# Optimization experiments

Measured on AMD Instinct MI355X. Metric: run time of the kernel, lower is better.

The kernel has to match this reference:

```python
import jax, jax.numpy as jnp
import numpy as np

H_SIZE = 2048
N_HEADS = 16
N_KV = 4
HEAD_DIM = 128
EPS = 1e-6
ROPE_THETA = 10000.0


def _rms_norm(x, w):
    # per-head RMSNorm over last dim (head_dim)
    var = jnp.mean(jnp.square(x), axis=-1, keepdims=True)
    return x * jax.lax.rsqrt(var + EPS) * w


def _rope(x, positions):
    # neox-style rotary over full head_dim. x: [B,S,H,D], positions: [B,S]
    d = x.shape[-1]
    inv_freq = 1.0 / (ROPE_THETA ** (jnp.arange(0, d, 2, dtype=jnp.float32) / d))
    ang = positions.astype(jnp.float32)[..., None] * inv_freq  # [B,S,D/2]
    cos = jnp.cos(ang)[:, :, None, :]
    sin = jnp.sin(ang)[:, :, None, :]
    x1, x2 = x[..., : d // 2], x[..., d // 2 :]
    return jnp.concatenate([x1 * cos - x2 * sin, x2 * cos + x1 * sin], axis=-1)


def setup_inputs() -> dict:
    key = jax.random.key(0)
    k1, k2, k3 = jax.random.split(key, 3)
    B, S = 2, 2048
    positions = jnp.broadcast_to(jnp.arange(S, dtype=jnp.int32), (B, S))
    hidden_states = jax.random.normal(k1, (B, S, H_SIZE), dtype=jnp.float32)
    w_qkv = jax.random.normal(k2, (H_SIZE, (N_HEADS + 2 * N_KV) * HEAD_DIM), dtype=jnp.float32) * 0.02
    w_o = jax.random.normal(k3, (N_HEADS * HEAD_DIM, H_SIZE), dtype=jnp.float32) * 0.02
    q_norm_w = jnp.ones((HEAD_DIM,), dtype=jnp.float32)
    k_norm_w = jnp.ones((HEAD_DIM,), dtype=jnp.float32)
    return {"positions": positions, "hidden_states": hidden_states, "w_qkv": w_qkv,
            "w_o": w_o, "q_norm_w": q_norm_w, "k_norm_w": k_norm_w}


def reference(positions, hidden_states, w_qkv, w_o, q_norm_w, k_norm_w):
    B, S, _ = hidden_states.shape
    q_size = N_HEADS * HEAD_DIM
    kv_size = N_KV * HEAD_DIM
    qkv = hidden_states @ w_qkv  # [B,S,q+2kv]
    q = qkv[..., :q_size].reshape(B, S, N_HEADS, HEAD_DIM)
    k = qkv[..., q_size : q_size + kv_size].reshape(B, S, N_KV, HEAD_DIM)
    v = qkv[..., q_size + kv_size :].reshape(B, S, N_KV, HEAD_DIM)
    q = _rms_norm(q, q_norm_w)
    k = _rms_norm(k, k_norm_w)
    q = _rope(q, positions)
    k = _rope(k, positions)
    # GQA: repeat kv heads
    rep = N_HEADS // N_KV
    k = jnp.repeat(k, rep, axis=2)
    v = jnp.repeat(v, rep, axis=2)
    scale = HEAD_DIM ** -0.5
    scores = jnp.einsum("bqhd,bkhd->bhqk", q, k) * scale
    causal = jnp.tril(jnp.ones((S, S), dtype=bool))
    scores = jnp.where(causal, scores, jnp.finfo(scores.dtype).min)
    probs = jax.nn.softmax(scores, axis=-1)
    attn = jnp.einsum("bhqk,bkhd->bqhd", probs, v).reshape(B, S, N_HEADS * HEAD_DIM)
    return attn @ w_o
```

## Files before the change

kernel.cpp:

```cpp
#include <hip/hip_runtime.h>
#include <math.h>

#define TOKS 4096
#define HS   2048
#define QKV_N 3072
#define S_LEN 2048
#define NH   16
#define NKV  4
#define DH   128

typedef __attribute__((ext_vector_type(8))) short short8;
typedef __attribute__((ext_vector_type(4))) float f32x4;

static __device__ __forceinline__ unsigned short f2bf(float f) {
  unsigned u = __builtin_bit_cast(unsigned, f);
  u += 0x7fffu + ((u >> 16) & 1u);
  return (unsigned short)(u >> 16);
}
static __device__ __forceinline__ float bf2f(unsigned short s) {
  unsigned u = (unsigned)s << 16;
  return __builtin_bit_cast(float, u);
}

__global__ __launch_bounds__(256)
void cvt_bf16(const float* __restrict__ in, unsigned short* __restrict__ out) {
  const size_t i = ((size_t)blockIdx.x * 256 + threadIdx.x) * 8;
  float4 a = *(const float4*)(in + i);
  float4 b = *(const float4*)(in + i + 4);
  short8 r;
  r[0] = f2bf(a.x); r[1] = f2bf(a.y); r[2] = f2bf(a.z); r[3] = f2bf(a.w);
  r[4] = f2bf(b.x); r[5] = f2bf(b.y); r[6] = f2bf(b.z); r[7] = f2bf(b.w);
  *(short8*)(out + i) = r;
}

__global__ __launch_bounds__(256)
void transpose_cvt(const float* __restrict__ in, unsigned short* __restrict__ out,
                   int R, int C, int ldin,
                   long in_z_hi, long in_z_lo, int z_mod, long out_z) {
  __shared__ float tile[32][33];
  const int z = blockIdx.z;
  in  += (size_t)(z / z_mod) * in_z_hi + (size_t)(z % z_mod) * in_z_lo;
  out += (size_t)z * out_z;
  const int r0 = blockIdx.x * 32, c0 = blockIdx.y * 32;
  const int tx = threadIdx.x & 31, ty = threadIdx.x >> 5;
  #pragma unroll
  for (int i = 0; i < 4; ++i)
    tile[ty + i * 8][tx] = in[(size_t)(r0 + ty + i * 8) * ldin + c0 + tx];
  __syncthreads();
  #pragma unroll
  for (int i = 0; i < 4; ++i)
    out[(size_t)(c0 + ty + i * 8) * R + r0 + tx] = f2bf(tile[tx][ty + i * 8]);
}

__global__ __launch_bounds__(256)
void transpose_bf16(const unsigned short* __restrict__ in, unsigned short* __restrict__ out,
                    int R, int C, int ldin,
                    long in_z_hi, long in_z_lo, int z_mod, long out_z) {
  __shared__ unsigned short tile[32][33];
  const int z = blockIdx.z;
  in  += (size_t)(z / z_mod) * in_z_hi + (size_t)(z % z_mod) * in_z_lo;
  out += (size_t)z * out_z;
  const int r0 = blockIdx.x * 32, c0 = blockIdx.y * 32;
  const int tx = threadIdx.x & 31, ty = threadIdx.x >> 5;
  #pragma unroll
  for (int i = 0; i < 4; ++i)
    tile[ty + i * 8][tx] = in[(size_t)(r0 + ty + i * 8) * ldin + c0 + tx];
  __syncthreads();
  #pragma unroll
  for (int i = 0; i < 4; ++i)
    out[(size_t)(c0 + ty + i * 8) * R + r0 + tx] = tile[tx][ty + i * 8];
}

__global__ __launch_bounds__(256)
void norm_rope_cvt(const unsigned short* __restrict__ qkv, const int* __restrict__ positions,
                   const float* __restrict__ qw, const float* __restrict__ kw,
                   unsigned short* __restrict__ Qb, unsigned short* __restrict__ Kb) {
  const int tok  = blockIdx.x;
  const int slot = blockIdx.y * 4 + (threadIdx.x >> 6);
  const int lane = threadIdx.x & 63;
  const int b = tok >> 11, s = tok & 2047;

  const unsigned short* x; const float* wgt; unsigned short* outp; float scale;
  if (slot < NH) {
    x = qkv + (size_t)tok * QKV_N + slot * DH;  wgt = qw;
    outp = Qb + (((size_t)b * NH + slot) * S_LEN + s) * DH;
    scale = 0.08838834764831845f;
  } else {
    const int kh = slot - NH;
    x = qkv + (size_t)tok * QKV_N + NH * DH + kh * DH;  wgt = kw;
    outp = Kb + (((size_t)b * NKV + kh) * S_LEN + s) * DH;
    scale = 1.0f;
  }

  float x1 = bf2f(x[lane]), x2 = bf2f(x[lane + 64]);
  float ss = x1 * x1 + x2 * x2;
  #pragma unroll
  for (int o = 32; o > 0; o >>= 1) ss += __shfl_xor(ss, o, 64);
  const float rs = 1.0f / sqrtf(ss * (1.0f / 128.0f) + 1e-6f);
  const float n1 = x1 * rs * wgt[lane];
  const float n2 = x2 * rs * wgt[lane + 64];

  const float pos = (float)positions[tok];
  const float inv_freq = exp2f(-(float)lane * (13.287712379549449f / 64.0f));
  float sn, cs;
  sincosf(pos * inv_freq, &sn, &cs);

  outp[lane]      = f2bf((n1 * cs - n2 * sn) * scale);
  outp[lane + 64] = f2bf((n2 * cs + n1 * sn) * scale);
}

template <int OUT_BF16, int NB>
__global__ __launch_bounds__(512, 2)
void gemm256(const unsigned short* __restrict__ A, const unsigned short* __restrict__ Bt,
             void* __restrict__ Cv, int M, int N, int K) {
  constexpr int NW   = NB / 4;
  constexpr int NACC = NB / 64;
  constexpr int BL   = NB / 128;

  __shared__ __align__(16) unsigned short LA[2][256 * 64];
  __shared__ __align__(16) unsigned short LB[2][NB * 64];

  const int t = threadIdx.x, w = t >> 6, l = t & 63;
  const int lm = l & 15, lr = l >> 4;
  const int wr = w >> 2, wc = w & 3;
  const int bn = blockIdx.x * NB, bm = blockIdx.y * 256;
  const int nkt = K >> 6;

  f32x4 acc[8][NACC];
  #pragma unroll
  for (int mi = 0; mi < 8; ++mi)
    #pragma unroll
    for (int ni = 0; ni < NACC; ++ni) acc[mi][ni] = {0.f, 0.f, 0.f, 0.f};

  auto stageA = [&](unsigned short* Lb, int half, int kt) {
    if (kt >= nkt) return;
    const int k0 = kt << 6;
    #pragma unroll
    for (int r = 0; r < 2; ++r) {
      const int row  = half * 128 + r * 64 + (t >> 3);
      const int slot = (t & 7) ^ (row & 7);
      const unsigned short* src = A + (size_t)(bm + row) * K + k0 + slot * 8;
      __builtin_amdgcn_global_load_lds(
          (const __attribute__((address_space(1))) void*)src,
          (__attribute__((address_space(3))) void*)(Lb + (half * 128 + r * 64 + w * 8) * 64),
          16, 0, 0);
    }
  };
  auto stageB = [&](unsigned short* Lb, int half, int kt) {
    if (kt >= nkt) return;
    const int k0 = kt << 6;
    #pragma unroll
    for (int r = 0; r < BL; ++r) {
      const int row  = half * (NB / 2) + r * 64 + (t >> 3);
      const int slot = (t & 7) ^ (row & 7);
      const unsigned short* src = Bt + (size_t)(bn + row) * K + k0 + slot * 8;
      __builtin_amdgcn_global_load_lds(
          (const __attribute__((address_space(1))) void*)src,
          (__attribute__((address_space(3))) void*)(Lb + (half * (NB / 2) + r * 64 + w * 8) * 64),
          16, 0, 0);
    }
  };

  stageB(&LB[0][0], 0, 0); stageB(&LB[0][0], 1, 0);
  stageA(&LA[0][0], 0, 0); stageA(&LA[0][0], 1, 0);
  stageB(&LB[1][0], 0, 1); stageB(&LB[1][0], 1, 1);
  if constexpr (NB == 256) asm volatile("s_waitcnt vmcnt(4)" ::: "memory");
  else                     asm volatile("s_waitcnt vmcnt(2)" ::: "memory");
  __builtin_amdgcn_s_barrier();

  const int niter = nkt >> 1;
  for (int i = 0; i < niter; ++i) {
    const int t0 = i * 2;
    short8 bfr[NACC][2];
    #pragma unroll
    for (int p = 0; p < 8; ++p) {
      const int buf = p >> 2, q = p & 3;
      const unsigned short* La = &LA[buf][0];
      const unsigned short* Lb = &LB[buf][0];

      if (q == 0) {
        #pragma unroll
        for (int ni = 0; ni < NACC; ++ni)
          #pragma unroll
          for (int ks = 0; ks < 2; ++ks) {
            const int row = wc * NW + ni * 16 + lm;
            bfr[ni][ks] = *(const short8*)(Lb + row * 64 +
                                           ((ks * 32 + lr * 8) ^ ((row & 7) << 3)));
          }
      }
      short8 af[2][2];
      #pragma unroll
      for (int mi2 = 0; mi2 < 2; ++mi2)
        #pragma unroll
        for (int ks = 0; ks < 2; ++ks) {
          const int row = wr * 128 + (q * 2 + mi2) * 16 + lm;
          af[mi2][ks] = *(const short8*)(La + row * 64 +
                                         ((ks * 32 + lr * 8) ^ ((row & 7) << 3)));
        }

      switch (p) {
        case 0: stageA(&LA[1][0], 0, t0 + 1); break;
        case 1: stageA(&LA[1][0], 1, t0 + 1); break;
        case 2: stageB(&LB[0][0], 0, t0 + 2); break;
        case 3: stageB(&LB[0][0], 1, t0 + 2); break;
        case 4: stageA(&LA[0][0], 0, t0 + 2); break;
        case 5: stageA(&LA[0][0], 1, t0 + 2); break;
        case 6: stageB(&LB[1][0], 0, t0 + 3); break;
        case 7: stageB(&LB[1][0], 1, t0 + 3); break;
      }

      __builtin_amdgcn_s_barrier();
      asm volatile("s_waitcnt lgkmcnt(0)" ::: "memory");
      __builtin_amdgcn_sched_barrier(0);

      __builtin_amdgcn_s_setprio(1);
      #pragma unroll
      for (int mi2 = 0; mi2 < 2; ++mi2)
        #pragma unroll
        for (int ni = 0; ni < NACC; ++ni)
          #pragma unroll
          for (int ks = 0; ks < 2; ++ks)
            acc[q * 2 + mi2][ni] = __builtin_amdgcn_mfma_f32_16x16x32_bf16(
                af[mi2][ks], bfr[ni][ks], acc[q * 2 + mi2][ni], 0, 0, 0);
      __builtin_amdgcn_s_setprio(0);

      if (q == 3) {
        if (i == niter - 1) asm volatile("s_waitcnt vmcnt(0)" ::: "memory");
        else if constexpr (NB == 256) asm volatile("s_waitcnt vmcnt(4)" ::: "memory");
        else                          asm volatile("s_waitcnt vmcnt(2)" ::: "memory");
      }
      __builtin_amdgcn_s_barrier();
    }
  }

  #pragma unroll
  for (int mi = 0; mi < 8; ++mi)
    #pragma unroll
    for (int ni = 0; ni < NACC; ++ni)
      #pragma unroll
      for (int j = 0; j < 4; ++j) {
        const size_t idx =
            (size_t)(bm + wr * 128 + mi * 16 + lr * 4 + j) * N + bn + wc * NW + ni * 16 + lm;
        if constexpr (OUT_BF16) ((unsigned short*)Cv)[idx] = f2bf(acc[mi][ni][j]);
        else                    ((float*)Cv)[idx] = acc[mi][ni][j];
      }
}

#define M_INIT 12.0f
#define P_CAP  2981.0f

__global__ __launch_bounds__(512)
void attn_mfma(const unsigned short* __restrict__ Qb, const unsigned short* __restrict__ Kb,
               const unsigned short* __restrict__ Vt, unsigned short* __restrict__ att) {
  __shared__ unsigned short Ks_[2][64 * 128];
  __shared__ unsigned short Vs_[2][128 * 64];
  __shared__ unsigned short Pl[8][16 * 64];

  const int x  = blockIdx.x;
  const int b  = blockIdx.z;
  const int qb = b ? x : 15 - x;
  const int h  = blockIdx.y;
  const int kvh = h >> 2;
  const int t = threadIdx.x, w = t >> 6, l = t & 63;
  const int lm = l & 15, lr = l >> 4;
  const int row0 = qb * 128 + w * 16;

  const unsigned short* qbase = Qb + ((size_t)(b * NH + h)) * S_LEN * DH;
  const unsigned short* kbase = Kb + ((size_t)(b * NKV + kvh)) * S_LEN * DH;
  const unsigned short* vtbase = Vt + ((size_t)(b * NKV + kvh)) * DH * S_LEN;

  short8 qf[4];
  #pragma unroll
  for (int kc = 0; kc < 4; ++kc)
    qf[kc] = *(const short8*)(qbase + (size_t)(row0 + lm) * DH + kc * 32 + lr * 8);

  short8 ones;
  #pragma unroll
  for (int i = 0; i < 8; ++i) ones[i] = (short)0x3F80;

  f32x4 o[8];
  #pragma unroll
  for (int ng = 0; ng < 8; ++ng) o[ng] = {0.f, 0.f, 0.f, 0.f};
  f32x4 lacc = {0.f, 0.f, 0.f, 0.f};
  float m_run[4];
  #pragma unroll
  for (int j = 0; j < 4; ++j) m_run[j] = M_INIT;

  auto stage = [&](int bufi, int kb0) {
    #pragma unroll
    for (int i = 0; i < 2; ++i) {
      const int rk = i * 32 + w * 4 + (l >> 4);
      const unsigned short* gk =
          kbase + (size_t)(kb0 + rk) * DH + (((l & 15) ^ (rk & 7)) * 8);
      __builtin_amdgcn_global_load_lds(
          (const __attribute__((address_space(1))) void*)gk,
          (__attribute__((address_space(3))) void*)(&Ks_[bufi][(i * 512 + w * 64) * 8]),
          16, 0, 0);
      const int rv = i * 64 + w * 8 + (l >> 3);
      const unsigned short* gv =
          vtbase + (size_t)rv * S_LEN + kb0 + (((l & 7) ^ (rv & 7)) * 8);
      __builtin_amdgcn_global_load_lds(
          (const __attribute__((address_space(1))) void*)gv,
          (__attribute__((address_space(3))) void*)(&Vs_[bufi][(i * 512 + w * 64) * 8]),
          16, 0, 0);
    }
  };

  const int nkt = qb * 2 + 2;
  stage(0, 0);
  __syncthreads();

  for (int kt = 0; kt < nkt; ++kt) {
    const int kb0 = kt * 64;
    if (kt + 1 < nkt) stage((kt + 1) & 1, kb0 + 64);

    if (kb0 <= row0 + 15) {
      const unsigned short* Kc = Ks_[kt & 1];
      const unsigned short* Vc = Vs_[kt & 1];
      const int rsw = (lm & 7) << 3;

      f32x4 s[4];
      #pragma unroll
      for (int n2 = 0; n2 < 4; ++n2) s[n2] = {0.f, 0.f, 0.f, 0.f};
      __builtin_amdgcn_s_setprio(1);
      #pragma unroll
      for (int n2 = 0; n2 < 4; ++n2) {
        #pragma unroll
        for (int kc = 0; kc < 4; ++kc) {
          const short8 kf = *(const short8*)(Kc + (n2 * 16 + lm) * 128 +
                                             ((kc * 32 + lr * 8) ^ rsw));
          s[n2] = __builtin_amdgcn_mfma_f32_16x16x32_bf16(qf[kc], kf, s[n2], 0, 0, 0);
        }
      }
      __builtin_amdgcn_s_setprio(0);

      if (kb0 + 63 > row0) {
        const int qi = row0 + lr * 4;
        #pragma unroll
        for (int n2 = 0; n2 < 4; ++n2) {
          const int kvi = kb0 + n2 * 16 + lm;
          #pragma unroll
          for (int j = 0; j < 4; ++j)
            if (kvi > qi + j) s[n2][j] = -1e30f;
        }
      }

      float pm = 0.f;
      #pragma unroll
      for (int n2 = 0; n2 < 4; ++n2)
        #pragma unroll
        for (int j = 0; j < 4; ++j) {
          const float p = __expf(s[n2][j] - m_run[j]);
          s[n2][j] = p;
          pm = fmaxf(pm, p);
        }

      if (!__all(pm <= P_CAP)) {
        #pragma unroll
        for (int j = 0; j < 4; ++j) {
          float v = fmaxf(fmaxf(s[0][j], s[1][j]), fmaxf(s[2][j], s[3][j]));
          v = fmaxf(v, __shfl_xor(v, 1, 64));
          v = fmaxf(v, __shfl_xor(v, 2, 64));
          v = fmaxf(v, __shfl_xor(v, 4, 64));
          v = fmaxf(v, __shfl_xor(v, 8, 64));
          if (v > P_CAP) {
            const float al = 1.0f / v;
            m_run[j] += __logf(v);
            lacc[j] *= al;
            #pragma unroll
            for (int n2 = 0; n2 < 4; ++n2) s[n2][j] *= al;
            #pragma unroll
            for (int ng = 0; ng < 8; ++ng) o[ng][j] *= al;
          }
        }
      }

      #pragma unroll
      for (int j = 0; j < 4; ++j) {
        const int prow = lr * 4 + j;
        unsigned short* Pw = &Pl[w][prow * 64];
        const int sw = (prow & 7) << 3;
        Pw[lm ^ sw]        = f2bf(s[0][j]);
        Pw[(16 + lm) ^ sw] = f2bf(s[1][j]);
        Pw[(32 + lm) ^ sw] = f2bf(s[2][j]);
        Pw[(48 + lm) ^ sw] = f2bf(s[3][j]);
      }
      __asm__ volatile("s_waitcnt lgkmcnt(0)" ::: "memory");

      short8 pf[2];
      #pragma unroll
      for (int k2 = 0; k2 < 2; ++k2)
        pf[k2] = *(const short8*)(&Pl[w][lm * 64 + ((k2 * 32 + lr * 8) ^ rsw)]);
      __builtin_amdgcn_s_setprio(1);
      lacc = __builtin_amdgcn_mfma_f32_16x16x32_bf16(pf[0], ones, lacc, 0, 0, 0);
      lacc = __builtin_amdgcn_mfma_f32_16x16x32_bf16(pf[1], ones, lacc, 0, 0, 0);
      #pragma unroll
      for (int ng = 0; ng < 8; ++ng) {
        const short8 vf0 = *(const short8*)(Vc + (ng * 16 + lm) * 64 + ((lr * 8) ^ rsw));
        const short8 vf1 = *(const short8*)(Vc + (ng * 16 + lm) * 64 + ((32 + lr * 8) ^ rsw));
        o[ng] = __builtin_amdgcn_mfma_f32_16x16x32_bf16(pf[0], vf0, o[ng], 0, 0, 0);
        o[ng] = __builtin_amdgcn_mfma_f32_16x16x32_bf16(pf[1], vf1, o[ng], 0, 0, 0);
      }
      __builtin_amdgcn_s_setprio(0);
    }
    __syncthreads();
  }

  #pragma unroll
  for (int j = 0; j < 4; ++j) {
    const float linv = 1.0f / lacc[j];
    unsigned short* ar =
        att + ((size_t)(b * S_LEN) + row0 + lr * 4 + j) * (NH * DH) + h * DH + lm;
    #pragma unroll
    for (int ng = 0; ng < 8; ++ng) ar[ng * 16] = f2bf(o[ng][j] * linv);
  }
}

extern "C" void kernel_launch(void* const* d_in, const int* in_sizes, int n_in,
                              void* d_out, int out_size, void* d_ws, size_t ws_size,
                              hipStream_t stream) {
  const int*   positions = (const int*)  d_in[0];
  const float* hidden    = (const float*)d_in[1];
  const float* w_qkv     = (const float*)d_in[2];
  const float* w_o       = (const float*)d_in[3];
  const float* q_norm_w  = (const float*)d_in[4];
  const float* k_norm_w  = (const float*)d_in[5];
  float* out = (float*)d_out;

  char* ws = (char*)d_ws;
  unsigned short* qkvb  = (unsigned short*)ws;
  unsigned short* att   = (unsigned short*)ws;
  char* region = ws + (size_t)TOKS * QKV_N * 4;
  unsigned short* hb    = (unsigned short*)region;
  unsigned short* Qb    = (unsigned short*)region;
  unsigned short* wqkvt = (unsigned short*)(region + 16777216);
  unsigned short* Kb    = (unsigned short*)(region + 16777216);
  unsigned short* Vt    = (unsigned short*)(region + 20971520);
  unsigned short* wot   = (unsigned short*)(region + 25165824);

  cvt_bf16<<<(TOKS * HS) / (256 * 8), 256, 0, stream>>>(hidden, hb);
  transpose_cvt<<<dim3(HS / 32, QKV_N / 32, 1), 256, 0, stream>>>(
      w_qkv, wqkvt, HS, QKV_N, QKV_N, 0, 0, 1, 0);
  gemm256<1, 256><<<dim3(QKV_N / 256, TOKS / 256), 512, 0, stream>>>(
      hb, wqkvt, qkvb, TOKS, QKV_N, HS);
  norm_rope_cvt<<<dim3(TOKS, 5), 256, 0, stream>>>(
      qkvb, positions, q_norm_w, k_norm_w, Qb, Kb);
  transpose_bf16<<<dim3(S_LEN / 32, DH / 32, 2 * NKV), 256, 0, stream>>>(
      qkvb + (NH + NKV) * DH, Vt, S_LEN, DH, QKV_N,
      (long)S_LEN * QKV_N, DH, NKV, (long)DH * S_LEN);
  transpose_cvt<<<dim3(HS / 32, HS / 32, 1), 256, 0, stream>>>(
      w_o, wot, HS, HS, HS, 0, 0, 1, 0);
  attn_mfma<<<dim3(16, NH, 2), 512, 0, stream>>>(Qb, Kb, Vt, att);
  gemm256<0, 128><<<dim3(HS / 128, TOKS / 256), 512, 0, stream>>>(
      att, wot, out, TOKS, HS, HS);
}
```

Baseline: 248.1 us.

## Split long causal attention query blocks across two workgroups with merge kernel

Query blocks 9-15 have their KV range split in half across two workgroups. Each half writes unnormalized partial outputs plus running max and sum to workspace, and a new merge kernel combines them with the log-sum-exp rescale. The point is to balance the causal triangle's uneven work so the longest blocks stop setting the attention kernel's tail. The cost is an extra launch, fp32 partial traffic and a larger grid (23x16x2).

```diff
diff --git a/kernel.cpp b/kernel.cpp
--- a/kernel.cpp
+++ b/kernel.cpp
@@ -251,18 +251,28 @@
 
 __global__ __launch_bounds__(512)
 void attn_mfma(const unsigned short* __restrict__ Qb, const unsigned short* __restrict__ Kb,
-               const unsigned short* __restrict__ Vt, unsigned short* __restrict__ att) {
+               const unsigned short* __restrict__ Vt, unsigned short* __restrict__ att,
+               float* __restrict__ Opart, float* __restrict__ LMpart) {
   __shared__ unsigned short Ks_[2][64 * 128];
   __shared__ unsigned short Vs_[2][128 * 64];
   __shared__ unsigned short Pl[8][16 * 64];
 
   const int x  = blockIdx.x;
+  const int h  = blockIdx.y;
   const int b  = blockIdx.z;
-  const int qb = b ? x : 15 - x;
-  const int h  = blockIdx.y;
   const int kvh = h >> 2;
   const int t = threadIdx.x, w = t >> 6, l = t & 63;
   const int lm = l & 15, lr = l >> 4;
+
+  int qb, k0t, k1t, pslot;
+  if (x == 0)       { qb = 8; k0t = 0; k1t = 18; pslot = -1; }
+  else if (x <= 14) {
+    const int s = x - 1;  qb = 15 - (s >> 1);
+    const int nk = 2 * qb + 2, mid = nk >> 1, half = s & 1;
+    k0t = half ? mid : 0;  k1t = half ? nk : mid;
+    pslot = ((b * NH + h) * 7 + (qb - 9)) * 2 + half;
+  } else            { qb = 22 - x; k0t = 0; k1t = 2 * qb + 2; pslot = -1; }
+
   const int row0 = qb * 128 + w * 16;
 
   const unsigned short* qbase = Qb + ((size_t)(b * NH + h)) * S_LEN * DH;
@@ -306,13 +316,12 @@
     }
   };
 
-  const int nkt = qb * 2 + 2;
-  stage(0, 0);
+  stage(k0t & 1, k0t * 64);
   __syncthreads();
 
-  for (int kt = 0; kt < nkt; ++kt) {
+  for (int kt = k0t; kt < k1t; ++kt) {
     const int kb0 = kt * 64;
-    if (kt + 1 < nkt) stage((kt + 1) & 1, kb0 + 64);
+    if (kt + 1 < k1t) stage((kt + 1) & 1, kb0 + 64);
 
     if (kb0 <= row0 + 15) {
       const unsigned short* Kc = Ks_[kt & 1];
@@ -406,13 +415,63 @@
     __syncthreads();
   }
 
-  #pragma unroll
-  for (int j = 0; j < 4; ++j) {
-    const float linv = 1.0f / lacc[j];
-    unsigned short* ar =
-        att + ((size_t)(b * S_LEN) + row0 + lr * 4 + j) * (NH * DH) + h * DH + lm;
-    #pragma unroll
-    for (int ng = 0; ng < 8; ++ng) ar[ng * 16] = f2bf(o[ng][j] * linv);
+  if (pslot < 0) {
+    #pragma unroll
+    for (int j = 0; j < 4; ++j) {
+      const float linv = 1.0f / lacc[j];
+      unsigned short* ar =
+          att + ((size_t)(b * S_LEN) + row0 + lr * 4 + j) * (NH * DH) + h * DH + lm;
+      #pragma unroll
+      for (int ng = 0; ng < 8; ++ng) ar[ng * 16] = f2bf(o[ng][j] * linv);
+    }
+  } else {
+    float* Po = Opart + (size_t)pslot * 16384;
+    #pragma unroll
+    for (int j = 0; j < 4; ++j) {
+      const int rl = w * 16 + lr * 4 + j;
+      #pragma unroll
+      for (int ng = 0; ng < 8; ++ng)
+        Po[rl * 128 + ng * 16 + lm] = o[ng][j];
+      if (lm == 0) {
+        LMpart[pslot * 256 + rl]       = lacc[j];
+        LMpart[pslot * 256 + 128 + rl] = m_run[j];
+      }
+    }
+  }
+}
+
+__global__ __launch_bounds__(256)
+void attn_merge(const float* __restrict__ Opart, const float* __restrict__ LMpart,
+                unsigned short* __restrict__ att) {
+  const int qs = blockIdx.x;
+  const int h  = blockIdx.y;
+  const int b  = blockIdx.z;
+  const int qb = 9 + qs;
+  const int sidx = (b * NH + h) * 7 + qs;
+  const int t = threadIdx.x;
+  const int r  = t >> 1;
+  const int c0 = (t & 1) * 64;
+
+  const float l0 = LMpart[(sidx * 2 + 0) * 256 + r];
+  const float m0 = LMpart[(sidx * 2 + 0) * 256 + 128 + r];
+  const float l1 = LMpart[(sidx * 2 + 1) * 256 + r];
+  const float m1 = LMpart[(sidx * 2 + 1) * 256 + 128 + r];
+  const float M  = fmaxf(m0, m1);
+  const float a0 = __expf(m0 - M), a1 = __expf(m1 - M);
+  const float linv = 1.0f / (l0 * a0 + l1 * a1);
+
+  const float* O0 = Opart + ((size_t)(sidx * 2 + 0) * 16384) + r * 128 + c0;
+  const float* O1 = Opart + ((size_t)(sidx * 2 + 1) * 16384) + r * 128 + c0;
+  unsigned short* ar =
+      att + ((size_t)(b * S_LEN) + qb * 128 + r) * (NH * DH) + h * DH + c0;
+  #pragma unroll
+  for (int i = 0; i < 16; ++i) {
+    float4 v0 = *(const float4*)(O0 + i * 4);
+    float4 v1 = *(const float4*)(O1 + i * 4);
+    ar[i * 4 + 0] = f2bf((v0.x * a0 + v1.x * a1) * linv);
+    ar[i * 4 + 1] = f2bf((v0.y * a0 + v1.y * a1) * linv);
+    ar[i * 4 + 2] = f2bf((v0.z * a0 + v1.z * a1) * linv);
+    ar[i * 4 + 3] = f2bf((v0.w * a0 + v1.w * a1) * linv);
   }
 }
 
@@ -430,6 +489,8 @@
   char* ws = (char*)d_ws;
   unsigned short* qkvb  = (unsigned short*)ws;
   unsigned short* att   = (unsigned short*)ws;
+  float* Opart  = (float*)(ws + 18874368);
+  float* LMpart = (float*)(ws + 18874368 + 29360128);
   char* region = ws + (size_t)TOKS * QKV_N * 4;
   unsigned short* hb    = (unsigned short*)region;
   unsigned short* Qb    = (unsigned short*)region;
@@ -450,7 +511,8 @@
       (long)S_LEN * QKV_N, DH, NKV, (long)DH * S_LEN);
   transpose_cvt<<<dim3(HS / 32, HS / 32, 1), 256, 0, stream>>>(
       w_o, wot, HS, HS, HS, 0, 0, 1, 0);
-  attn_mfma<<<dim3(16, NH, 2), 512, 0, stream>>>(Qb, Kb, Vt, att);
+  attn_mfma<<<dim3(23, NH, 2), 512, 0, stream>>>(Qb, Kb, Vt, att, Opart, LMpart);
+  attn_merge<<<dim3(7, NH, 2), 256, 0, stream>>>(Opart, LMpart, att);
   gemm256<0, 128><<<dim3(HS / 128, TOKS / 256), 512, 0, stream>>>(
       att, wot, out, TOKS, HS, HS);
 }
```

Result: slower. 258.4 us (+4.1%).
